# Kernel optimization log

Measured on AMD Instinct MI355X. Metric: run time of the kernel, lower is better.

## Reference

```python
import jax, jax.numpy as jnp
from jax import lax
import numpy as np

NUM_CLASSES = 6
WIN = 11


def setup_inputs() -> dict:
    key = jax.random.key(0)
    k1, k2 = jax.random.split(key)
    x = jax.random.normal(k1, (8, NUM_CLASSES, 512, 512), dtype=jnp.float32)
    target = jax.random.randint(k2, (8, 1, 512, 512), 0, NUM_CLASSES, dtype=jnp.int32)
    return {"x": x, "target": target}


def reference(x, target):
    # log-softmax over class dim
    log_p = jax.nn.log_softmax(x, axis=1)  # [B,C,H,W]

    w = -jnp.ones((1, 1, WIN, WIN), dtype=jnp.float32)
    w = w.at[0, 0, WIN // 2, WIN // 2].set(float(WIN * WIN - 1))
    t = target.astype(jnp.float32)  # [B,1,H,W]
    edge = lax.conv_general_dilated(
        t, w, window_strides=(1, 1), padding='SAME',
        dimension_numbers=('NCHW', 'OIHW', 'NCHW'))
    edge_mask = (edge != 0).astype(jnp.float32)  # [B,1,H,W], binarized

    # dynamic smoothing = fraction of edge pixels, capped at 0.2
    s = jnp.minimum(jnp.mean(edge_mask), jnp.float32(0.2))

    labels = target[:, 0]  # [B,H,W]
    onehot = jax.nn.one_hot(labels, NUM_CLASSES, axis=1, dtype=jnp.float32)  # [B,C,H,W]
    # to_categorical(alpha=s): alpha off-class, 1 - alpha + alpha/C on-class
    soft = s * (1.0 - onehot) + (1.0 - s + s / NUM_CLASSES) * onehot

    mask = onehot * (1.0 - edge_mask) + soft * edge_mask  # [B,C,H,W]
    loss = jnp.mean(jnp.sum(mask * log_p, axis=1))
    return -loss
```

## Files before the change

kernel.cpp:

```cpp
#include <hip/hip_runtime.h>

#define BATCH   8
#define NCLS    6
#define HW      512
#define IMGPIX  (HW * HW)
#define NPIX    (BATCH * IMGPIX)
#define TILE    32
#define HALO    5
#define SM      (TILE + 2 * HALO)
#define RSTRIDE 36
#define NB      (BATCH * 256)

__device__ __forceinline__ float get4(const float4& v, int j) {
    return j == 0 ? v.x : j == 1 ? v.y : j == 2 ? v.z : v.w;
}

__global__ __launch_bounds__(256, 4) void ls_main_kernel(
        const float* __restrict__ x,
        const int*   __restrict__ tgt,
        float4*      __restrict__ part) {
    __shared__ int   s_t[SM * SM];
    __shared__ int   s_rs[SM][RSTRIDE];
    __shared__ float sw1[4], sw2[4];
    __shared__ int   swe[4];

    const int tid  = threadIdx.x;
    const int blk  = blockIdx.x;
    const int b    = blk & 7;
    const int tile = blk >> 3;
    const int tr   = (tile >> 4) * TILE;
    const int tc   = (tile & 15) * TILE;

    const int* timg = tgt + b * IMGPIX;

    int tv[7];
#pragma unroll
    for (int i = 0; i < 7; i++) {
        const int e  = tid + i * 256;
        const int ly = e / SM;
        const int lx = e - ly * SM;
        int v = 0;
        if (e < SM * SM) {
            const int gy = tr - HALO + ly, gx = tc - HALO + lx;
            if (gy >= 0 && gy < HW && gx >= 0 && gx < HW) v = timg[gy * HW + gx];
        }
        tv[i] = v;
    }

    const int py = tid >> 3;
    const int px = (tid & 7) << 2;
    const int gy = tr + py;
    const int gx = tc + px;
    const float* xb = x + ((size_t)(b * NCLS) << 18) + (gy << 9) + gx;
    float4 xc[NCLS];
#pragma unroll
    for (int c = 0; c < NCLS; c++)
        xc[c] = *(const float4*)(xb + ((size_t)c << 18));

#pragma unroll
    for (int i = 0; i < 7; i++) {
        const int e = tid + i * 256;
        if (e < SM * SM) s_t[e] = tv[i];
    }
    __syncthreads();

    if (tid < SM * 4) {
        const int row  = tid >> 2;
        const int c0   = (tid & 3) << 3;
        const int base = row * SM + c0;
        int buf[18];
#pragma unroll
        for (int k = 0; k < 18; k++) buf[k] = s_t[base + k];
        int acc = 0;
#pragma unroll
        for (int k = 0; k < 11; k++) acc += buf[k];
        s_rs[row][c0] = acc;
#pragma unroll
        for (int k = 1; k < 8; k++) {
            acc += buf[k + 10] - buf[k - 1];
            s_rs[row][c0 + k] = acc;
        }
    }
    __syncthreads();

    int4 bs = make_int4(0, 0, 0, 0);
#pragma unroll
    for (int dy = 0; dy <= 2 * HALO; dy++) {
        const int4 r = *(const int4*)&s_rs[py + dy][px];
        bs.x += r.x; bs.y += r.y; bs.z += r.z; bs.w += r.w;
    }
    const int bsa[4] = {bs.x, bs.y, bs.z, bs.w};
    int t4a[4];
#pragma unroll
    for (int j = 0; j < 4; j++) t4a[j] = s_t[(py + HALO) * SM + px + HALO + j];

    float r1 = 0.f, r2 = 0.f;
    int ec = 0;
#pragma unroll
    for (int j = 0; j < 4; j++) {
        const float a0 = get4(xc[0], j), a1 = get4(xc[1], j), a2 = get4(xc[2], j);
        const float a3 = get4(xc[3], j), a4 = get4(xc[4], j), a5 = get4(xc[5], j);
        const float se = __expf(a0) + __expf(a1) + __expf(a2) +
                         __expf(a3) + __expf(a4) + __expf(a5);
        const float lse = __logf(se);
        const int   t   = t4a[j];
        const float xt  = t == 0 ? a0 : t == 1 ? a1 : t == 2 ? a2 :
                          t == 3 ? a3 : t == 4 ? a4 : a5;
        const float lpl = xt - lse;
        r1 += lpl;
        const int ev = 121 * t - bsa[j];
        const int eb = (ev != 0) ? 1 : 0;
        const float S = (a0 + a1 + a2 + a3 + a4 + a5) - 6.f * lse;
        r2 = fmaf((float)eb, S - (11.0f / 6.0f) * lpl, r2);
        ec += eb;
    }

#pragma unroll
    for (int off = 32; off > 0; off >>= 1) {
        r1 += __shfl_down(r1, off);
        r2 += __shfl_down(r2, off);
        ec += __shfl_down(ec, off);
    }
    const int wave = tid >> 6;
    if ((tid & 63) == 0) { sw1[wave] = r1; sw2[wave] = r2; swe[wave] = ec; }
    __syncthreads();
    if (tid == 0) {
        part[blk] = make_float4(sw1[0] + sw1[1] + sw1[2] + sw1[3],
                                sw2[0] + sw2[1] + sw2[2] + sw2[3],
                                (float)(swe[0] + swe[1] + swe[2] + swe[3]),
                                0.f);
    }
}

__global__ __launch_bounds__(256) void ls_finalize_kernel(
        const float4* __restrict__ part,
        float* __restrict__ out) {
    const int tid = threadIdx.x;
    double d1 = 0.0, d2 = 0.0, de = 0.0;
#pragma unroll
    for (int i = 0; i < NB / 256; i++) {
        const float4 p = part[tid + i * 256];
        d1 += (double)p.x;
        d2 += (double)p.y;
        de += (double)p.z;
    }
#pragma unroll
    for (int off = 32; off > 0; off >>= 1) {
        d1 += __shfl_down(d1, off);
        d2 += __shfl_down(d2, off);
        de += __shfl_down(de, off);
    }
    __shared__ double sd1[4], sd2[4], sde[4];
    const int wave = tid >> 6;
    if ((tid & 63) == 0) { sd1[wave] = d1; sd2[wave] = d2; sde[wave] = de; }
    __syncthreads();
    if (tid == 0) {
        const double R1 = sd1[0] + sd1[1] + sd1[2] + sd1[3];
        const double R2 = sd2[0] + sd2[1] + sd2[2] + sd2[3];
        const double E  = sde[0] + sde[1] + sde[2] + sde[3];
        const float  s  = fminf((float)E * (1.0f / (float)NPIX), 0.2f);
        const double loss = (R1 + (double)s * R2) * (1.0 / (double)NPIX);
        out[0] = (float)(-loss);
    }
}

extern "C" void kernel_launch(void* const* d_in, const int* in_sizes, int n_in,
                              void* d_out, int out_size, void* d_ws, size_t ws_size,
                              hipStream_t stream) {
    const float* x   = (const float*)d_in[0];
    const int*   tgt = (const int*)d_in[1];
    float*       out = (float*)d_out;
    float4*      part = (float4*)d_ws;

    ls_main_kernel<<<NB, 256, 0, stream>>>(x, tgt, part);
    ls_finalize_kernel<<<1, 256, 0, stream>>>(part, out);
}
```

Before: 88.81 us.

## Process two horizontal tiles per block with prefetched loads for the second tile

Each block now handles two adjacent 32x32 tiles, which halves the grid. Loads of target and logits for the second tile are issued up front so they are in flight while the first tile's box filter and softmax run. This gives more memory parallelism per thread and fewer block launches and partial sums. In exchange it raises register pressure (twelve float4 plus two target arrays), adds barriers, and halves the number of blocks available to fill the GPU.

After: 93.89 us. 5.7% more time.

```diff
diff --git a/kernel.cpp b/kernel.cpp
--- a/kernel.cpp
+++ b/kernel.cpp
@@ -9,7 +9,7 @@
 #define HALO    5
 #define SM      (TILE + 2 * HALO)
 #define RSTRIDE 36
-#define NB      (BATCH * 256)
+#define NB      (BATCH * 128)
 
 __device__ __forceinline__ float get4(const float4& v, int j) {
     return j == 0 ? v.x : j == 1 ? v.y : j == 2 ? v.z : v.w;
@@ -24,16 +24,17 @@
     __shared__ float sw1[4], sw2[4];
     __shared__ int   swe[4];
 
-    const int tid  = threadIdx.x;
-    const int blk  = blockIdx.x;
-    const int b    = blk & 7;
-    const int tile = blk >> 3;
-    const int tr   = (tile >> 4) * TILE;
-    const int tc   = (tile & 15) * TILE;
+    const int tid = threadIdx.x;
+    const int blk = blockIdx.x;
+    const int b   = blk & 7;
+    const int tp  = blk >> 3;
+    const int tr  = (tp >> 3) * TILE;
+    const int tc0 = (tp & 7) * (2 * TILE);
+    const int tc1 = tc0 + TILE;
 
     const int* timg = tgt + b * IMGPIX;
 
-    int tv[7];
+    int tva[7];
 #pragma unroll
     for (int i = 0; i < 7; i++) {
         const int e  = tid + i * 256;
@@ -41,26 +42,46 @@
         const int lx = e - ly * SM;
         int v = 0;
         if (e < SM * SM) {
-            const int gy = tr - HALO + ly, gx = tc - HALO + lx;
+            const int gy = tr - HALO + ly, gx = tc0 - HALO + lx;
             if (gy >= 0 && gy < HW && gx >= 0 && gx < HW) v = timg[gy * HW + gx];
         }
-        tv[i] = v;
+        tva[i] = v;
     }
 
     const int py = tid >> 3;
     const int px = (tid & 7) << 2;
-    const int gy = tr + py;
-    const int gx = tc + px;
-    const float* xb = x + ((size_t)(b * NCLS) << 18) + (gy << 9) + gx;
+    const float* xr = x + ((size_t)(b * NCLS) << 18) + ((size_t)(tr + py) << 9);
     float4 xc[NCLS];
 #pragma unroll
     for (int c = 0; c < NCLS; c++)
-        xc[c] = *(const float4*)(xb + ((size_t)c << 18));
+        xc[c] = *(const float4*)(xr + ((size_t)c << 18) + (tc0 + px));
+
+    int tvb[7];
+#pragma unroll
+    for (int i = 0; i < 7; i++) {
+        const int e  = tid + i * 256;
+        const int ly = e / SM;
+        const int lx = e - ly * SM;
+        int v = 0;
+        if (e < SM * SM) {
+            const int gy = tr - HALO + ly, gx = tc1 - HALO + lx;
+            if (gy >= 0 && gy < HW && gx >= 0 && gx < HW) v = timg[gy * HW + gx];
+        }
+        tvb[i] = v;
+    }
+
+    float4 xd[NCLS];
+#pragma unroll
+    for (int c = 0; c < NCLS; c++)
+        xd[c] = *(const float4*)(xr + ((size_t)c << 18) + (tc1 + px));
+
+    float r1 = 0.f, r2 = 0.f;
+    int   ec = 0;
 
 #pragma unroll
     for (int i = 0; i < 7; i++) {
         const int e = tid + i * 256;
-        if (e < SM * SM) s_t[e] = tv[i];
+        if (e < SM * SM) s_t[e] = tva[i];
     }
     __syncthreads();
 
@@ -83,19 +104,24 @@
     }
     __syncthreads();
 
-    int4 bs = make_int4(0, 0, 0, 0);
+    int4 bs0 = make_int4(0, 0, 0, 0);
 #pragma unroll
     for (int dy = 0; dy <= 2 * HALO; dy++) {
         const int4 r = *(const int4*)&s_rs[py + dy][px];
-        bs.x += r.x; bs.y += r.y; bs.z += r.z; bs.w += r.w;
-    }
-    const int bsa[4] = {bs.x, bs.y, bs.z, bs.w};
+        bs0.x += r.x; bs0.y += r.y; bs0.z += r.z; bs0.w += r.w;
+    }
+    const int bsa[4] = {bs0.x, bs0.y, bs0.z, bs0.w};
     int t4a[4];
 #pragma unroll
     for (int j = 0; j < 4; j++) t4a[j] = s_t[(py + HALO) * SM + px + HALO + j];
-
-    float r1 = 0.f, r2 = 0.f;
-    int ec = 0;
+    __syncthreads();
+
+#pragma unroll
+    for (int i = 0; i < 7; i++) {
+        const int e = tid + i * 256;
+        if (e < SM * SM) s_t[e] = tvb[i];
+    }
+
 #pragma unroll
     for (int j = 0; j < 4; j++) {
         const float a0 = get4(xc[0], j), a1 = get4(xc[1], j), a2 = get4(xc[2], j);
@@ -114,6 +140,56 @@
         r2 = fmaf((float)eb, S - (11.0f / 6.0f) * lpl, r2);
         ec += eb;
     }
+    __syncthreads();
+
+    if (tid < SM * 4) {
+        const int row  = tid >> 2;
+        const int c0   = (tid & 3) << 3;
+        const int base = row * SM + c0;
+        int buf[18];
+#pragma unroll
+        for (int k = 0; k < 18; k++) buf[k] = s_t[base + k];
+        int acc = 0;
+#pragma unroll
+        for (int k = 0; k < 11; k++) acc += buf[k];
+        s_rs[row][c0] = acc;
+#pragma unroll
+        for (int k = 1; k < 8; k++) {
+            acc += buf[k + 10] - buf[k - 1];
+            s_rs[row][c0 + k] = acc;
+        }
+    }
+    __syncthreads();
+
+    int4 bs1 = make_int4(0, 0, 0, 0);
+#pragma unroll
+    for (int dy = 0; dy <= 2 * HALO; dy++) {
+        const int4 r = *(const int4*)&s_rs[py + dy][px];
+        bs1.x += r.x; bs1.y += r.y; bs1.z += r.z; bs1.w += r.w;
+    }
+    const int bsb[4] = {bs1.x, bs1.y, bs1.z, bs1.w};
+    int t4b[4];
+#pragma unroll
+    for (int j = 0; j < 4; j++) t4b[j] = s_t[(py + HALO) * SM + px + HALO + j];
+
+#pragma unroll
+    for (int j = 0; j < 4; j++) {
+        const float a0 = get4(xd[0], j), a1 = get4(xd[1], j), a2 = get4(xd[2], j);
+        const float a3 = get4(xd[3], j), a4 = get4(xd[4], j), a5 = get4(xd[5], j);
+        const float se = __expf(a0) + __expf(a1) + __expf(a2) +
+                         __expf(a3) + __expf(a4) + __expf(a5);
+        const float lse = __logf(se);
+        const int   t   = t4b[j];
+        const float xt  = t == 0 ? a0 : t == 1 ? a1 : t == 2 ? a2 :
+                          t == 3 ? a3 : t == 4 ? a4 : a5;
+        const float lpl = xt - lse;
+        r1 += lpl;
+        const int ev = 121 * t - bsb[j];
+        const int eb = (ev != 0) ? 1 : 0;
+        const float S = (a0 + a1 + a2 + a3 + a4 + a5) - 6.f * lse;
+        r2 = fmaf((float)eb, S - (11.0f / 6.0f) * lpl, r2);
+        ec += eb;
+    }
 
 #pragma unroll
     for (int off = 32; off > 0; off >>= 1) {
```
